# Kernel tuning notes

Measured on AMD Instinct MI355X. Metric: run time of the kernel, lower is better.

Reference implementation:

```python
import jax, jax.numpy as jnp
import numpy as np

PROP_TIME = 1  # matches cspn = Affinity_Propagate(prop_time=1)
# torch ZeroPad2d (left,right,top,bottom) rewritten as ((top,bottom),(left,right)) per gate 1..8
PADS = [((0, 2), (0, 2)), ((0, 2), (1, 1)), ((0, 2), (2, 0)),
        ((1, 1), (0, 2)), ((1, 1), (2, 0)),
        ((2, 0), (0, 2)), ((2, 0), (1, 1)), ((2, 0), (2, 0))]


def _pad8(x):
    # x: (B, C, H, W) -> (B, 8, C, H+2, W+2): the 8 shifted/zero-padded neighbor maps
    return jnp.stack([jnp.pad(x, ((0, 0), (0, 0), pt, pl)) for pt, pl in PADS], axis=1)


def _affinity_norm(g):
    # g: (B, 8, H, W) -> gate_wb (B, 8, H+2, W+2), gate_sum (B, H, W)
    gate_wb = jnp.stack([jnp.pad(g[:, k], ((0, 0), pt, pl))
                         for k, (pt, pl) in enumerate(PADS)], axis=1)
    abs_w = jnp.sum(jnp.abs(gate_wb), axis=1, keepdims=True)  # sum_conv(|gate_wb|)
    gate_wb = gate_wb / abs_w
    gate_sum = jnp.sum(gate_wb, axis=1)[:, 1:-1, 1:-1]
    return gate_wb, gate_sum


def _prop_once(gate_wb, gate_sum, blur):
    # blur: (B, C, H, W); gate_wb broadcasts over channel dim C
    nws = jnp.sum(gate_wb[:, :, None] * _pad8(blur), axis=1)[:, :, 1:-1, 1:-1]
    return (1.0 - gate_sum[:, None]) * blur + nws  # '8sum' norm


def setup_inputs() -> dict:
    key = jax.random.key(0)
    k1, k2 = jax.random.split(key)
    guidance = jax.random.normal(k1, (24, 128, 128, 16), dtype=jnp.float32)
    blur = jax.random.normal(k2, (20, 128, 128, 16), dtype=jnp.float32)
    return {"guidance": guidance, "blur": blur}


def reference(guidance, blur):
    # guidance: (24, H, W, Z); blur: (C, H, W, Z)
    gwx, gsx = _affinity_norm(jnp.transpose(guidance[0:8], (3, 0, 1, 2)))    # (Z,8,H,W)
    gwy, gsy = _affinity_norm(jnp.transpose(guidance[8:16], (2, 0, 1, 3)))   # (W,8,H,Z)
    gwz, gsz = _affinity_norm(jnp.transpose(guidance[16:24], (1, 0, 2, 3)))  # (H,8,W,Z)
    result = blur
    for _ in range(PROP_TIME):
        result = jnp.transpose(_prop_once(gwx, gsx, jnp.transpose(result, (3, 0, 1, 2))), (1, 2, 3, 0))
        result = jnp.transpose(_prop_once(gwy, gsy, jnp.transpose(result, (2, 0, 1, 3))), (1, 2, 0, 3))
        result = jnp.transpose(_prop_once(gwz, gsz, jnp.transpose(result, (1, 0, 2, 3))), (1, 0, 2, 3))
    return result
```

## Files before the change

kernel.cpp:

```cpp
#include <hip/hip_runtime.h>

#define H 128
#define W 128
#define Zd 16
#define C 20
#define HWZ (H * W * Zd)

#define CG 5
#define CPG (C / CG)
#define POSBLOCKS 256
#define NXCD 8

#define CGF 4
#define CPGF (C / CGF)

typedef float f4 __attribute__((ext_vector_type(4)));

__device__ __forceinline__ f4 load4(const float* p) { return *(const f4*)p; }
__device__ __forceinline__ f4 load4u(const float* p) {
    f4 r;
    __builtin_memcpy(&r, p, 16);
    return r;
}

__device__ __forceinline__ void decode(int bid, int tidx, int& cg, int& tid) {
    int xcd = bid & (NXCD - 1);
    int i = bid >> 3;
    cg = i >> 5;
    int pb = (xcd << 5) + (i & 31);
    tid = pb * 256 + tidx;
}

__global__ __launch_bounds__(256) void prop_x(const float* __restrict__ gd,
                                              const float* __restrict__ in,
                                              float* __restrict__ out) {
    int cg, tid;
    decode(blockIdx.x, threadIdx.x, cg, tid);
    const int z4 = (tid & 3) << 2;
    const int w = (tid >> 2) & (W - 1);
    const int h = tid >> 9;

    const int DI[8] = {1, 1, 1, 0, 0, -1, -1, -1};
    const int DJ[8] = {1, 0, -1, 1, -1, 1, 0, -1};

    f4 g[8];
    int noff[8];
    f4 A = {0, 0, 0, 0}, S = {0, 0, 0, 0};
#pragma unroll
    for (int k = 0; k < 8; ++k) {
        int hh = h + DI[k], ww = w + DJ[k];
        bool valid = ((unsigned)hh < H) && ((unsigned)ww < W);
        f4 val = {0, 0, 0, 0};
        if (valid) val = load4(gd + ((k * H + hh) * W + ww) * Zd + z4);
        g[k] = val;
        noff[k] = valid ? (DI[k] * W + DJ[k]) * Zd : 0;
#pragma unroll
        for (int e = 0; e < 4; ++e) A[e] += __builtin_fabsf(val[e]);
        S += val;
    }
    f4 invA = 1.0f / A;
    f4 c0 = 1.0f - S * invA;
#pragma unroll
    for (int k = 0; k < 8; ++k) g[k] *= invA;

    const int base = (h * W + w) * Zd + z4;
#pragma unroll
    for (int cc = 0; cc < CPG; ++cc) {
        const int c = cg * CPG + cc;
        const float* pc = in + c * HWZ + base;
        f4 acc = c0 * load4(pc);
#pragma unroll
        for (int k = 0; k < 8; ++k) acc += g[k] * load4(pc + noff[k]);
        *(f4*)(out + c * HWZ + base) = acc;
    }
}

__global__ __launch_bounds__(512) void prop_yz(const float* __restrict__ gd,
                                               const float* __restrict__ in,
                                               float* __restrict__ out) {
    const int bid = blockIdx.x;
    const int xcd = bid & (NXCD - 1);
    const int i = bid >> 3;
    const int cgf = i >> 4;
    const int h = (xcd << 4) + (i & 15);

    const int t = threadIdx.x;
    const int z4 = (t & 3) << 2;
    const int w = t >> 2;

    __shared__ float yout[CPGF][W][Zd];

    const int DI[8] = {1, 1, 1, 0, 0, -1, -1, -1};
    const int DJ[8] = {1, 0, -1, 1, -1, 1, 0, -1};
    const int base = (h * W + w) * Zd + z4;
    const int loo = (z4 == 0) ? 0 : -1;
    const int hio = (z4 == 12) ? 3 : 4;

    {
        const int gbase = (((8 * H) + h) * W + w) * Zd + z4;
        f4 g[8];
        f4 A = {0, 0, 0, 0}, S = {0, 0, 0, 0};
#pragma unroll
        for (int k = 0; k < 8; ++k) {
            int di = DI[k], dj = DJ[k];
            bool rv = (unsigned)(h + di) < H;
            f4 val = {0, 0, 0, 0};
            if (rv) {
                val = (dj == 0) ? load4(gd + gbase + k * HWZ + di * (W * Zd))
                                : load4u(gd + gbase + k * HWZ + di * (W * Zd) + dj);
                if (dj == -1 && z4 == 0) val[0] = 0.f;
                if (dj == 1 && z4 == 12) val[3] = 0.f;
            }
            g[k] = val;
#pragma unroll
            for (int e = 0; e < 4; ++e) A[e] += __builtin_fabsf(val[e]);
            S += val;
        }
        f4 invA = 1.0f / A;
        f4 c0 = 1.0f - S * invA;
#pragma unroll
        for (int k = 0; k < 8; ++k) g[k] *= invA;

        f4 gp[3] = {g[0], g[3], g[5]};
        f4 gc[3] = {g[1], c0, g[6]};
        f4 gm[3] = {g[2], g[4], g[7]};
        const int DIr[3] = {1, 0, -1};
        int rowoff[3];
#pragma unroll
        for (int r = 0; r < 3; ++r)
            rowoff[r] = ((unsigned)(h + DIr[r]) < H) ? DIr[r] * (W * Zd) : 0;

#pragma unroll
        for (int cc = 0; cc < CPGF; ++cc) {
            const int c = cgf * CPGF + cc;
            const float* pc = in + c * HWZ + base;
            f4 acc = {0, 0, 0, 0};
#pragma unroll
            for (int r = 0; r < 3; ++r) {
                const float* pr = pc + rowoff[r];
                f4 v = load4(pr);
                float lo = pr[loo];
                float hi = pr[hio];
                f4 tm = {lo, v[0], v[1], v[2]};
                f4 tp = {v[1], v[2], v[3], hi};
                acc += gm[r] * tm + gc[r] * v + gp[r] * tp;
            }
            *(f4*)(&yout[cc][w][z4]) = acc;
        }
    }

    __syncthreads();

    {
        const int gbase = (((16 * H) + h) * W + w) * Zd + z4;
        f4 g[8];
        f4 A = {0, 0, 0, 0}, S = {0, 0, 0, 0};
#pragma unroll
        for (int k = 0; k < 8; ++k) {
            int di = DI[k], dj = DJ[k];
            bool rv = (unsigned)(w + di) < W;
            f4 val = {0, 0, 0, 0};
            if (rv) {
                val = (dj == 0) ? load4(gd + gbase + k * HWZ + di * Zd)
                                : load4u(gd + gbase + k * HWZ + di * Zd + dj);
                if (dj == -1 && z4 == 0) val[0] = 0.f;
                if (dj == 1 && z4 == 12) val[3] = 0.f;
            }
            g[k] = val;
#pragma unroll
            for (int e = 0; e < 4; ++e) A[e] += __builtin_fabsf(val[e]);
            S += val;
        }
        f4 invA = 1.0f / A;
        f4 c0 = 1.0f - S * invA;
#pragma unroll
        for (int k = 0; k < 8; ++k) g[k] *= invA;

        f4 gp[3] = {g[0], g[3], g[5]};
        f4 gc[3] = {g[1], c0, g[6]};
        f4 gm[3] = {g[2], g[4], g[7]};
        const int DIr[3] = {1, 0, -1};
        int woff[3];
#pragma unroll
        for (int r = 0; r < 3; ++r)
            woff[r] = ((unsigned)(w + DIr[r]) < W) ? DIr[r] * Zd : 0;

#pragma unroll
        for (int cc = 0; cc < CPGF; ++cc) {
            const int c = cgf * CPGF + cc;
            const float* pl = &yout[cc][w][z4];
            f4 acc = {0, 0, 0, 0};
#pragma unroll
            for (int r = 0; r < 3; ++r) {
                const float* pr = pl + woff[r];
                f4 v = load4(pr);
                float lo = pr[loo];
                float hi = pr[hio];
                f4 tm = {lo, v[0], v[1], v[2]};
                f4 tp = {v[1], v[2], v[3], hi};
                acc += gm[r] * tm + gc[r] * v + gp[r] * tp;
            }
            *(f4*)(out + c * HWZ + base) = acc;
        }
    }
}

extern "C" void kernel_launch(void* const* d_in, const int* in_sizes, int n_in,
                              void* d_out, int out_size, void* d_ws, size_t ws_size,
                              hipStream_t stream) {
    const float* gd = (const float*)d_in[0];
    const float* blur = (const float*)d_in[1];
    float* out = (float*)d_out;
    float* ws = (float*)d_ws;

    prop_x<<<dim3(POSBLOCKS * CG), dim3(256), 0, stream>>>(gd, blur, ws);
    prop_yz<<<dim3(512), dim3(512), 0, stream>>>(gd, ws, out);
}
```

Baseline: 33.70 us.

## Store y-pass intermediate in bf16 LDS and regroup channel work per block

prop_x now launches 256 blocks, each covering all 20 channels for a half row, so the 8 guidance gates are loaded and normalized once per position instead of five times. prop_yz now launches 256 blocks with 10 channels each and keeps its shared-memory intermediate in bf16, which halves LDS per channel so twice the channels fit per block and gate recomputation drops. The bf16 rounding reduces accuracy of the y-pass output before the z pass. Fewer, larger blocks may also lower occupancy and latency hiding.

```diff
diff --git a/kernel.cpp b/kernel.cpp
--- a/kernel.cpp
+++ b/kernel.cpp
@@ -5,14 +5,7 @@
 #define Zd 16
 #define C 20
 #define HWZ (H * W * Zd)
-
-#define CG 5
-#define CPG (C / CG)
-#define POSBLOCKS 256
 #define NXCD 8
-
-#define CGF 4
-#define CPGF (C / CGF)
 
 typedef float f4 __attribute__((ext_vector_type(4)));
 
@@ -22,23 +15,29 @@
     __builtin_memcpy(&r, p, 16);
     return r;
 }
-
-__device__ __forceinline__ void decode(int bid, int tidx, int& cg, int& tid) {
-    int xcd = bid & (NXCD - 1);
-    int i = bid >> 3;
-    cg = i >> 5;
-    int pb = (xcd << 5) + (i & 31);
-    tid = pb * 256 + tidx;
+__device__ __forceinline__ float bf2f(unsigned short u) {
+    unsigned v = ((unsigned)u) << 16;
+    float f;
+    __builtin_memcpy(&f, &v, 4);
+    return f;
+}
+__device__ __forceinline__ unsigned short f2bf(float f) {
+    unsigned u;
+    __builtin_memcpy(&u, &f, 4);
+    u = (u + 0x7fff + ((u >> 16) & 1)) >> 16;
+    return (unsigned short)u;
 }
 
 __global__ __launch_bounds__(256) void prop_x(const float* __restrict__ gd,
                                               const float* __restrict__ in,
                                               float* __restrict__ out) {
-    int cg, tid;
-    decode(blockIdx.x, threadIdx.x, cg, tid);
-    const int z4 = (tid & 3) << 2;
-    const int w = (tid >> 2) & (W - 1);
-    const int h = tid >> 9;
+    const int bid = blockIdx.x;
+    const int xcd = bid & (NXCD - 1);
+    const int i = bid >> 3;
+    const int h = (xcd << 4) + (i >> 1);
+    const int t = threadIdx.x;
+    const int z4 = (t & 3) << 2;
+    const int w = ((i & 1) << 6) + (t >> 2);
 
     const int DI[8] = {1, 1, 1, 0, 0, -1, -1, -1};
     const int DJ[8] = {1, 0, -1, 1, -1, 1, 0, -1};
@@ -64,9 +63,8 @@
     for (int k = 0; k < 8; ++k) g[k] *= invA;
 
     const int base = (h * W + w) * Zd + z4;
-#pragma unroll
-    for (int cc = 0; cc < CPG; ++cc) {
-        const int c = cg * CPG + cc;
+#pragma unroll 5
+    for (int c = 0; c < C; ++c) {
         const float* pc = in + c * HWZ + base;
         f4 acc = c0 * load4(pc);
 #pragma unroll
@@ -75,20 +73,21 @@
     }
 }
 
+#define CPGF 10
 __global__ __launch_bounds__(512) void prop_yz(const float* __restrict__ gd,
                                                const float* __restrict__ in,
                                                float* __restrict__ out) {
     const int bid = blockIdx.x;
     const int xcd = bid & (NXCD - 1);
     const int i = bid >> 3;
-    const int cgf = i >> 4;
-    const int h = (xcd << 4) + (i & 15);
+    const int cg = i & 1;
+    const int h = (xcd << 4) + (i >> 1);
 
     const int t = threadIdx.x;
     const int z4 = (t & 3) << 2;
     const int w = t >> 2;
 
-    __shared__ float yout[CPGF][W][Zd];
+    __shared__ unsigned short yout[CPGF][W][Zd];
 
     const int DI[8] = {1, 1, 1, 0, 0, -1, -1, -1};
     const int DJ[8] = {1, 0, -1, 1, -1, 1, 0, -1};
@@ -130,9 +129,9 @@
         for (int r = 0; r < 3; ++r)
             rowoff[r] = ((unsigned)(h + DIr[r]) < H) ? DIr[r] * (W * Zd) : 0;
 
-#pragma unroll
+#pragma unroll 2
         for (int cc = 0; cc < CPGF; ++cc) {
-            const int c = cgf * CPGF + cc;
+            const int c = cg * CPGF + cc;
             const float* pc = in + c * HWZ + base;
             f4 acc = {0, 0, 0, 0};
 #pragma unroll
@@ -145,7 +144,12 @@
                 f4 tp = {v[1], v[2], v[3], hi};
                 acc += gm[r] * tm + gc[r] * v + gp[r] * tp;
             }
-            *(f4*)(&yout[cc][w][z4]) = acc;
+            unsigned short us[4];
+#pragma unroll
+            for (int e = 0; e < 4; ++e) us[e] = f2bf(acc[e]);
+            unsigned long long packed;
+            __builtin_memcpy(&packed, us, 8);
+            *(unsigned long long*)(&yout[cc][w][z4]) = packed;
         }
     }
 
@@ -185,17 +189,17 @@
         for (int r = 0; r < 3; ++r)
             woff[r] = ((unsigned)(w + DIr[r]) < W) ? DIr[r] * Zd : 0;
 
-#pragma unroll
+#pragma unroll 2
         for (int cc = 0; cc < CPGF; ++cc) {
-            const int c = cgf * CPGF + cc;
-            const float* pl = &yout[cc][w][z4];
+            const int c = cg * CPGF + cc;
+            const unsigned short* pl = &yout[cc][w][z4];
             f4 acc = {0, 0, 0, 0};
 #pragma unroll
             for (int r = 0; r < 3; ++r) {
-                const float* pr = pl + woff[r];
-                f4 v = load4(pr);
-                float lo = pr[loo];
-                float hi = pr[hio];
+                const unsigned short* pr = pl + woff[r];
+                f4 v = {bf2f(pr[0]), bf2f(pr[1]), bf2f(pr[2]), bf2f(pr[3])};
+                float lo = bf2f(pr[loo]);
+                float hi = bf2f(pr[hio]);
                 f4 tm = {lo, v[0], v[1], v[2]};
                 f4 tp = {v[1], v[2], v[3], hi};
                 acc += gm[r] * tm + gc[r] * v + gp[r] * tp;
@@ -213,6 +217,6 @@
     float* out = (float*)d_out;
     float* ws = (float*)d_ws;
 
-    prop_x<<<dim3(POSBLOCKS * CG), dim3(256), 0, stream>>>(gd, blur, ws);
-    prop_yz<<<dim3(512), dim3(512), 0, stream>>>(gd, ws, out);
-}
+    prop_x<<<dim3(256), dim3(256), 0, stream>>>(gd, blur, ws);
+    prop_yz<<<dim3(256), dim3(512), 0, stream>>>(gd, ws, out);
+}
```

Result: slower. 41.92 us (+24.4%).

## Share x-gate normalization across channel groups via LDS in prop_x

Applied to the files above, without the earlier changes.

prop_x is restructured so that each block covers one row segment of 16 w positions across all four channel groups. One wavefront loads and normalizes the 8 x-direction gates and writes them to shared memory, and the other threads read them after a barrier. Before, each of the 5 channel-group blocks reloaded and renormalized the same gates. The change cuts that redundant gate traffic and arithmetic but adds a barrier and a phase where only one wave of the block is working. A launch-bounds occupancy hint is also added.

```diff
diff --git a/kernel.cpp b/kernel.cpp
--- a/kernel.cpp
+++ b/kernel.cpp
@@ -5,14 +5,7 @@
 #define Zd 16
 #define C 20
 #define HWZ (H * W * Zd)
-
-#define CG 5
-#define CPG (C / CG)
-#define POSBLOCKS 256
 #define NXCD 8
-
-#define CGF 4
-#define CPGF (C / CGF)
 
 typedef float f4 __attribute__((ext_vector_type(4)));
 
@@ -23,58 +16,74 @@
     return r;
 }
 
-__device__ __forceinline__ void decode(int bid, int tidx, int& cg, int& tid) {
-    int xcd = bid & (NXCD - 1);
-    int i = bid >> 3;
-    cg = i >> 5;
-    int pb = (xcd << 5) + (i & 31);
-    tid = pb * 256 + tidx;
-}
-
-__global__ __launch_bounds__(256) void prop_x(const float* __restrict__ gd,
-                                              const float* __restrict__ in,
-                                              float* __restrict__ out) {
-    int cg, tid;
-    decode(blockIdx.x, threadIdx.x, cg, tid);
-    const int z4 = (tid & 3) << 2;
-    const int w = (tid >> 2) & (W - 1);
-    const int h = tid >> 9;
+__global__ __launch_bounds__(256, 6) void prop_x(const float* __restrict__ gd,
+                                                 const float* __restrict__ in,
+                                                 float* __restrict__ out) {
+    const int bid = blockIdx.x;
+    const int xcd = bid & (NXCD - 1);
+    const int j = bid >> 3;
+    const int h = (xcd << 4) + (j >> 3);
+    const int wbase = (j & 7) << 4;
+
+    const int t = threadIdx.x;
+    const int p = t & 63;
+    const int cg = t >> 6;
+    const int z4 = (p & 3) << 2;
+    const int w = wbase + (p >> 2);
 
     const int DI[8] = {1, 1, 1, 0, 0, -1, -1, -1};
     const int DJ[8] = {1, 0, -1, 1, -1, 1, 0, -1};
 
-    f4 g[8];
+    __shared__ f4 xg[9][64];
+
+    if (t < 64) {
+        f4 g[8];
+        f4 A = {0, 0, 0, 0}, S = {0, 0, 0, 0};
+#pragma unroll
+        for (int k = 0; k < 8; ++k) {
+            int hh = h + DI[k], ww = w + DJ[k];
+            bool valid = ((unsigned)hh < H) && ((unsigned)ww < W);
+            f4 val = {0, 0, 0, 0};
+            if (valid) val = load4(gd + ((k * H + hh) * W + ww) * Zd + z4);
+            g[k] = val;
+#pragma unroll
+            for (int e = 0; e < 4; ++e) A[e] += __builtin_fabsf(val[e]);
+            S += val;
+        }
+        f4 invA = 1.0f / A;
+        f4 c0 = 1.0f - S * invA;
+#pragma unroll
+        for (int k = 0; k < 8; ++k) xg[k][t] = g[k] * invA;
+        xg[8][t] = c0;
+    }
+    __syncthreads();
+
+    f4 g[8], c0v;
+#pragma unroll
+    for (int k = 0; k < 8; ++k) g[k] = xg[k][p];
+    c0v = xg[8][p];
+
     int noff[8];
-    f4 A = {0, 0, 0, 0}, S = {0, 0, 0, 0};
 #pragma unroll
     for (int k = 0; k < 8; ++k) {
         int hh = h + DI[k], ww = w + DJ[k];
         bool valid = ((unsigned)hh < H) && ((unsigned)ww < W);
-        f4 val = {0, 0, 0, 0};
-        if (valid) val = load4(gd + ((k * H + hh) * W + ww) * Zd + z4);
-        g[k] = val;
         noff[k] = valid ? (DI[k] * W + DJ[k]) * Zd : 0;
-#pragma unroll
-        for (int e = 0; e < 4; ++e) A[e] += __builtin_fabsf(val[e]);
-        S += val;
-    }
-    f4 invA = 1.0f / A;
-    f4 c0 = 1.0f - S * invA;
-#pragma unroll
-    for (int k = 0; k < 8; ++k) g[k] *= invA;
+    }
 
     const int base = (h * W + w) * Zd + z4;
 #pragma unroll
-    for (int cc = 0; cc < CPG; ++cc) {
-        const int c = cg * CPG + cc;
+    for (int cc = 0; cc < 5; ++cc) {
+        const int c = cg * 5 + cc;
         const float* pc = in + c * HWZ + base;
-        f4 acc = c0 * load4(pc);
+        f4 acc = c0v * load4(pc);
 #pragma unroll
         for (int k = 0; k < 8; ++k) acc += g[k] * load4(pc + noff[k]);
         *(f4*)(out + c * HWZ + base) = acc;
     }
 }
 
+#define CPGF 5
 __global__ __launch_bounds__(512) void prop_yz(const float* __restrict__ gd,
                                                const float* __restrict__ in,
                                                float* __restrict__ out) {
@@ -213,6 +222,6 @@
     float* out = (float*)d_out;
     float* ws = (float*)d_ws;
 
-    prop_x<<<dim3(POSBLOCKS * CG), dim3(256), 0, stream>>>(gd, blur, ws);
+    prop_x<<<dim3(1024), dim3(256), 0, stream>>>(gd, blur, ws);
     prop_yz<<<dim3(512), dim3(512), 0, stream>>>(gd, ws, out);
 }
```

Measured after the change: 35.27 us. +4.6%, slower.
